# Kernel optimization log

Measured on AMD Instinct MI355X. Metric: run time of the kernel, lower is better.

## Reference

```python
import jax, jax.numpy as jnp
import numpy as np

H = 1024          # hidden_size
I = 2048          # intermediate_size (per routed expert; shared uses I*num_shared)
E = 8             # num_routed_experts
B, S = 2, 1024


def setup_inputs() -> dict:
    key = jax.random.key(0)
    ks = jax.random.split(key, 8)
    sc_h = 1.0 / np.sqrt(H)
    sc_i = 1.0 / np.sqrt(I)
    return {
        "hidden_states": jax.random.normal(ks[0], (B, S, H), jnp.float32),
        "gate_w": jax.random.normal(ks[1], (H, E), jnp.float32) * sc_h,      # router
        "sh_gate": jax.random.normal(ks[2], (H, I), jnp.float32) * sc_h,     # shared SwiGLU
        "sh_up": jax.random.normal(ks[3], (H, I), jnp.float32) * sc_h,
        "sh_down": jax.random.normal(ks[4], (I, H), jnp.float32) * sc_i,
        "rt_gate": jax.random.normal(ks[5], (E, H, I), jnp.float32) * sc_h,  # stacked routed experts
        "rt_up": jax.random.normal(ks[6], (E, H, I), jnp.float32) * sc_h,
        "rt_down": jax.random.normal(ks[7], (E, I, H), jnp.float32) * sc_i,
    }


def _swiglu(x, wg, wu, wd):
    return (jax.nn.silu(x @ wg) * (x @ wu)) @ wd


def reference(hidden_states, gate_w, sh_gate, sh_up, sh_down, rt_gate, rt_up, rt_down):
    b, s, h = hidden_states.shape
    x = hidden_states.reshape(-1, h)                      # [T, H]
    logits = x @ gate_w                                   # [T, E]
    # top-1 routing: score = sigmoid(max logit), expert = argmax
    top_val = jnp.max(logits, axis=-1, keepdims=True)     # [T, 1]
    top_id = jnp.argmax(logits, axis=-1)                  # [T]
    score = jax.nn.sigmoid(top_val)
    xs = x * score                                        # scale tokens BEFORE expert (Llama4)
    # exact dense-masked equivalent of sort/dispatch/per-expert SwiGLU/scatter-combine:
    # every expert is applied to all tokens, then the one-hot mask selects the
    # assigned expert's output per token (identical math to ragged dispatch).
    g = jnp.einsum('th,ehi->eti', xs, rt_gate)            # [E, T, I]
    u = jnp.einsum('th,ehi->eti', xs, rt_up)
    act = jax.nn.silu(g) * u
    y = jnp.einsum('eti,eih->eth', act, rt_down)          # [E, T, H]
    onehot = jax.nn.one_hot(top_id, E, dtype=x.dtype)     # [T, E]
    routed = jnp.einsum('eth,te->th', y, onehot)          # [T, H]
    shared = _swiglu(x, sh_gate, sh_up, sh_down)          # [T, H]
    return (shared + routed).reshape(b, s, h)
```

## Files before the change

kernel.cpp:

```cpp
#include <hip/hip_runtime.h>
#include <cstdint>
#include <cstddef>

#define T_TOK 2048
#define HDIM  1024
#define IDIM  2048
#define NEXP  8

#define BM 128
#define BK 32
#define BN2 64
#define MAXPAD 3072
#define SH_TILES 16
#define RT_TILES 24

typedef __attribute__((ext_vector_type(8))) short short8;
typedef __attribute__((ext_vector_type(4))) short short4v;
typedef __attribute__((ext_vector_type(4))) float float4v;

__device__ __forceinline__ short f2bf(float f) {
  uint32_t u = __float_as_uint(f);
  u += 0x7fffu + ((u >> 16) & 1u);
  return (short)(u >> 16);
}

__device__ __forceinline__ void gload_lds16(const void* g, void* l) {
  __builtin_amdgcn_global_load_lds(
      (const __attribute__((address_space(1))) uint32_t*)g,
      (__attribute__((address_space(3))) uint32_t*)l, 16, 0, 0);
}

__device__ __forceinline__ int swz(int c) { return c ^ ((c >> 4) & 3); }


__global__ __launch_bounds__(256) void zero_init(int* __restrict__ counts,
                                                 int* __restrict__ perm) {
  int i = threadIdx.x;
  if (i < NEXP) counts[i] = 0;
  for (int p = i; p < MAXPAD; p += 256) perm[p] = 0;
}

__global__ __launch_bounds__(256) void router_kernel(
    const float* __restrict__ x, const float* __restrict__ gw,
    short* __restrict__ xbf, short* __restrict__ xsbf,
    int* __restrict__ expert_id, int* __restrict__ slot,
    int* __restrict__ counts) {
  int wv = threadIdx.x >> 6, lane = threadIdx.x & 63;
  int t = blockIdx.x * 4 + wv;
  const float* xr = x + (size_t)t * HDIM;
  float4v xv[4];
  float lg[NEXP];
#pragma unroll
  for (int e = 0; e < NEXP; e++) lg[e] = 0.f;
#pragma unroll
  for (int p = 0; p < 4; p++) {
    xv[p] = *(const float4v*)(xr + p * 256 + lane * 4);
#pragma unroll
    for (int c = 0; c < 4; c++) {
      int h = p * 256 + lane * 4 + c;
      float4v g0 = *(const float4v*)(gw + (size_t)h * NEXP);
      float4v g1 = *(const float4v*)(gw + (size_t)h * NEXP + 4);
      float xc = xv[p][c];
      lg[0] += xc * g0[0]; lg[1] += xc * g0[1];
      lg[2] += xc * g0[2]; lg[3] += xc * g0[3];
      lg[4] += xc * g1[0]; lg[5] += xc * g1[1];
      lg[6] += xc * g1[2]; lg[7] += xc * g1[3];
    }
  }
#pragma unroll
  for (int ofs = 1; ofs < 64; ofs <<= 1) {
#pragma unroll
    for (int e = 0; e < NEXP; e++) lg[e] += __shfl_xor(lg[e], ofs, 64);
  }
  int be = 0;
  float bv = lg[0];
#pragma unroll
  for (int e = 1; e < NEXP; e++) {
    if (lg[e] > bv) { bv = lg[e]; be = e; }
  }
  float score = 1.f / (1.f + __expf(-bv));
  if (lane == 0) {
    expert_id[t] = be;
    slot[t] = atomicAdd(&counts[be], 1);
  }
#pragma unroll
  for (int p = 0; p < 4; p++) {
    short4v b, bs;
#pragma unroll
    for (int c = 0; c < 4; c++) {
      b[c] = f2bf(xv[p][c]);
      bs[c] = f2bf(xv[p][c] * score);
    }
    *(short4v*)(xbf + (size_t)t * HDIM + p * 256 + lane * 4) = b;
    *(short4v*)(xsbf + (size_t)t * HDIM + p * 256 + lane * 4) = bs;
  }
}

__global__ void prefix_kernel(const int* __restrict__ counts, int* __restrict__ pad_off) {
  if (threadIdx.x == 0 && blockIdx.x == 0) {
    int run = 0;
    for (int e = 0; e < NEXP; e++) {
      pad_off[e] = run;
      run += (counts[e] + BM - 1) & ~(BM - 1);
    }
    pad_off[NEXP] = run;
  }
}

__global__ __launch_bounds__(256) void build_perm(
    const int* __restrict__ expert_id, const int* __restrict__ slot,
    const int* __restrict__ pad_off, int* __restrict__ perm) {
  int t = blockIdx.x * 256 + threadIdx.x;
  int e = expert_id[t];
  perm[pad_off[e] + slot[t]] = t;
}


__global__ __launch_bounds__(256) void transpose_w1(
    const float* __restrict__ shg, const float* __restrict__ shu,
    const float* __restrict__ rtg, const float* __restrict__ rtu,
    short* __restrict__ shg_t, short* __restrict__ shu_t,
    short* __restrict__ rtg_t, short* __restrict__ rtu_t) {
  __shared__ __align__(16) short t[64][66];
  int z = blockIdx.z;
  const float *s0, *s1;
  short *d0, *d1;
  if (z == 0) { s0 = shg; s1 = shu; d0 = shg_t; d1 = shu_t; }
  else {
    size_t o = (size_t)(z - 1) * HDIM * IDIM;
    s0 = rtg + o; s1 = rtu + o; d0 = rtg_t + o; d1 = rtu_t + o;
  }
  const int R = HDIM, C = IDIM;
  int r0 = blockIdx.y * 64, c0 = blockIdx.x * 64;
  int tid = threadIdx.x;
  int tr = tid >> 4, tc = (tid & 15) * 4;
  int oc = tid >> 2, rs = (tid & 3) * 16;
#pragma unroll
  for (int pass = 0; pass < 2; pass++) {
    const float* s = pass ? s1 : s0;
    short* d = pass ? d1 : d0;
    if (pass) __syncthreads();
#pragma unroll
    for (int i = 0; i < 4; i++) {
      float4v v = *(const float4v*)(s + (size_t)(r0 + tr + i * 16) * C + c0 + tc);
      int w0 = (int)(unsigned short)f2bf(v[0]) | ((int)f2bf(v[1]) << 16);
      int w1 = (int)(unsigned short)f2bf(v[2]) | ((int)f2bf(v[3]) << 16);
      int* p = (int*)&t[tr + i * 16][tc];
      p[0] = w0;
      p[1] = w1;
    }
    __syncthreads();
    short8 o0, o1;
#pragma unroll
    for (int j = 0; j < 8; j++) { o0[j] = t[rs + j][oc]; o1[j] = t[rs + 8 + j][oc]; }
    short* dp = d + (size_t)(c0 + oc) * R + r0 + rs;
    *(short8*)dp = o0;
    *(short8*)(dp + 8) = o1;
  }
}

__global__ __launch_bounds__(256) void transpose_w2(
    const float* __restrict__ shd, const float* __restrict__ rtd,
    short* __restrict__ shd_t, short* __restrict__ rtd_t) {
  __shared__ __align__(16) short t[64][66];
  int z = blockIdx.z;
  const float* s = (z == 0) ? shd : rtd + (size_t)(z - 1) * IDIM * HDIM;
  short* d = (z == 0) ? shd_t : rtd_t + (size_t)(z - 1) * IDIM * HDIM;
  const int R = IDIM, C = HDIM;
  int r0 = blockIdx.y * 64, c0 = blockIdx.x * 64;
  int tid = threadIdx.x;
  int tr = tid >> 4, tc = (tid & 15) * 4;
  int oc = tid >> 2, rs = (tid & 3) * 16;
#pragma unroll
  for (int i = 0; i < 4; i++) {
    float4v v = *(const float4v*)(s + (size_t)(r0 + tr + i * 16) * C + c0 + tc);
    int w0 = (int)(unsigned short)f2bf(v[0]) | ((int)f2bf(v[1]) << 16);
    int w1 = (int)(unsigned short)f2bf(v[2]) | ((int)f2bf(v[3]) << 16);
    int* p = (int*)&t[tr + i * 16][tc];
    p[0] = w0;
    p[1] = w1;
  }
  __syncthreads();
  short8 o0, o1;
#pragma unroll
  for (int j = 0; j < 8; j++) { o0[j] = t[rs + j][oc]; o1[j] = t[rs + 8 + j][oc]; }
  short* dp = d + (size_t)(c0 + oc) * R + r0 + rs;
  *(short8*)dp = o0;
  *(short8*)(dp + 8) = o1;
}


__global__ __launch_bounds__(256) void gemm1_swiglu(
    const short* __restrict__ xbf, const short* __restrict__ xsbf,
    const short* __restrict__ shg_t, const short* __restrict__ shu_t,
    const short* __restrict__ rtg_t, const short* __restrict__ rtu_t,
    short* __restrict__ act_sh, short* __restrict__ act_rt,
    const int* __restrict__ pad_off, const int* __restrict__ perm) {
  __shared__ __align__(1024) short sA[BM * BK];
  __shared__ __align__(1024) short sBg[BM * BK];
  __shared__ __align__(1024) short sBu[BM * BK];
  int tid = threadIdx.x, lane = tid & 63, wv = tid >> 6;
  int C0 = blockIdx.x * 128;
  int y = blockIdx.y;
  const short *A, *Bg, *Bu;
  short* act;
  int R0;
  bool routed = (y >= SH_TILES);
  if (!routed) {
    A = xbf; Bg = shg_t; Bu = shu_t; act = act_sh; R0 = y * BM;
  } else {
    R0 = (y - SH_TILES) * BM;
    if (R0 >= pad_off[NEXP]) return;
    int e = 0;
    while (pad_off[e + 1] <= R0) e++;
    size_t o = (size_t)e * HDIM * IDIM;
    A = xsbf; Bg = rtg_t + o; Bu = rtu_t + o; act = act_rt;
  }
  int c0 = swz(tid), c1 = swz(tid + 256);
  int r0c = c0 >> 2, r1c = c1 >> 2;
  int ar0 = routed ? perm[R0 + r0c] : R0 + r0c;
  int ar1 = routed ? perm[R0 + r1c] : R0 + r1c;
  size_t gA0 = (size_t)ar0 * HDIM + (c0 & 3) * 8;
  size_t gA1 = (size_t)ar1 * HDIM + (c1 & 3) * 8;
  size_t gB0 = (size_t)(C0 + r0c) * HDIM + (c0 & 3) * 8;
  size_t gB1 = (size_t)(C0 + r1c) * HDIM + (c1 & 3) * 8;
  short* lds0 = (short*)nullptr;
  (void)lds0;
  short* lA0 = sA + tid * 8;  short* lA1 = sA + (tid + 256) * 8;
  short* lG0 = sBg + tid * 8; short* lG1 = sBg + (tid + 256) * 8;
  short* lU0 = sBu + tid * 8; short* lU1 = sBu + (tid + 256) * 8;

  float4v accg[4][4], accu[4][4];
  float4v z4 = {0.f, 0.f, 0.f, 0.f};
#pragma unroll
  for (int i = 0; i < 4; i++)
#pragma unroll
    for (int j = 0; j < 4; j++) { accg[i][j] = z4; accu[i][j] = z4; }

  const int wrow = (wv >> 1) * 64, wcol = (wv & 1) * 64;
  const int mrow = lane & 15, h4 = lane >> 4;
  int aoff[4], boff[4];
#pragma unroll
  for (int i = 0; i < 4; i++)
    aoff[i] = swz(((wrow + i * 16 + mrow) << 2) + h4) * 8;
#pragma unroll
  for (int j = 0; j < 4; j++)
    boff[j] = swz(((wcol + j * 16 + mrow) << 2) + h4) * 8;

  for (int k0 = 0; k0 < HDIM; k0 += BK) {
    __syncthreads();
    gload_lds16(A + gA0 + k0, lA0);
    gload_lds16(A + gA1 + k0, lA1);
    gload_lds16(Bg + gB0 + k0, lG0);
    gload_lds16(Bg + gB1 + k0, lG1);
    gload_lds16(Bu + gB0 + k0, lU0);
    gload_lds16(Bu + gB1 + k0, lU1);
    __syncthreads();
    short8 af[4], bg[4], bu[4];
#pragma unroll
    for (int i = 0; i < 4; i++) af[i] = *(const short8*)(sA + aoff[i]);
#pragma unroll
    for (int j = 0; j < 4; j++) {
      bg[j] = *(const short8*)(sBg + boff[j]);
      bu[j] = *(const short8*)(sBu + boff[j]);
    }
#pragma unroll
    for (int i = 0; i < 4; i++)
#pragma unroll
      for (int j = 0; j < 4; j++) {
        accg[i][j] = __builtin_amdgcn_mfma_f32_16x16x32_bf16(af[i], bg[j], accg[i][j], 0, 0, 0);
        accu[i][j] = __builtin_amdgcn_mfma_f32_16x16x32_bf16(af[i], bu[j], accu[i][j], 0, 0, 0);
      }
  }
  int qrow = h4 * 4, col = mrow;
#pragma unroll
  for (int i = 0; i < 4; i++)
#pragma unroll
    for (int j = 0; j < 4; j++)
#pragma unroll
      for (int r = 0; r < 4; r++) {
        int row = R0 + wrow + i * 16 + qrow + r;
        int c = C0 + wcol + j * 16 + col;
        float g = accg[i][j][r], u = accu[i][j][r];
        float sv = g / (1.f + __expf(-g)) * u;
        act[(size_t)row * IDIM + c] = f2bf(sv);
      }
}


__global__ __launch_bounds__(256) void gemm2_down(
    const short* __restrict__ act_sh, const short* __restrict__ act_rt,
    const short* __restrict__ shd_t, const short* __restrict__ rtd_t,
    float* __restrict__ out, float* __restrict__ rt_out,
    const int* __restrict__ pad_off, const int* __restrict__ counts,
    const int* __restrict__ perm) {
  __shared__ __align__(1024) short sA[BM * BK];
  __shared__ __align__(1024) short sB[BN2 * BK];
  int tid = threadIdx.x, lane = tid & 63, wv = tid >> 6;
  int C0 = blockIdx.x * BN2;
  int y = blockIdx.y;
  const short *A, *Bd;
  int R0, e = 0;
  bool routed = (y >= SH_TILES);
  if (!routed) {
    A = act_sh; Bd = shd_t; R0 = y * BM;
  } else {
    R0 = (y - SH_TILES) * BM;
    if (R0 >= pad_off[NEXP]) return;
    while (pad_off[e + 1] <= R0) e++;
    A = act_rt; Bd = rtd_t + (size_t)e * IDIM * HDIM;
  }
  int c0 = swz(tid), c1 = swz(tid + 256);
  size_t gA0 = (size_t)(R0 + (c0 >> 2)) * IDIM + (c0 & 3) * 8;
  size_t gA1 = (size_t)(R0 + (c1 >> 2)) * IDIM + (c1 & 3) * 8;
  size_t gB0 = (size_t)(C0 + (c0 >> 2)) * IDIM + (c0 & 3) * 8;
  short* lA0 = sA + tid * 8;
  short* lA1 = sA + (tid + 256) * 8;
  short* lB0 = sB + tid * 8;

  float4v acc[2][4];
  float4v z4 = {0.f, 0.f, 0.f, 0.f};
#pragma unroll
  for (int i = 0; i < 2; i++)
#pragma unroll
    for (int j = 0; j < 4; j++) acc[i][j] = z4;

  const int wrow = wv * 32;
  const int mrow = lane & 15, h4 = lane >> 4;
  int aoff[2], boff[4];
#pragma unroll
  for (int i = 0; i < 2; i++)
    aoff[i] = swz(((wrow + i * 16 + mrow) << 2) + h4) * 8;
#pragma unroll
  for (int j = 0; j < 4; j++)
    boff[j] = swz(((j * 16 + mrow) << 2) + h4) * 8;

  for (int k0 = 0; k0 < IDIM; k0 += BK) {
    __syncthreads();
    gload_lds16(A + gA0 + k0, lA0);
    gload_lds16(A + gA1 + k0, lA1);
    gload_lds16(Bd + gB0 + k0, lB0);
    __syncthreads();
    short8 af[2], bf4[4];
#pragma unroll
    for (int i = 0; i < 2; i++) af[i] = *(const short8*)(sA + aoff[i]);
#pragma unroll
    for (int j = 0; j < 4; j++) bf4[j] = *(const short8*)(sB + boff[j]);
#pragma unroll
    for (int i = 0; i < 2; i++)
#pragma unroll
      for (int j = 0; j < 4; j++)
        acc[i][j] = __builtin_amdgcn_mfma_f32_16x16x32_bf16(af[i], bf4[j], acc[i][j], 0, 0, 0);
  }
  int qrow = h4 * 4, col = mrow;
#pragma unroll
  for (int i = 0; i < 2; i++)
#pragma unroll
    for (int j = 0; j < 4; j++)
#pragma unroll
      for (int r = 0; r < 4; r++) {
        int row = R0 + wrow + i * 16 + qrow + r;
        int c = C0 + j * 16 + col;
        float v = acc[i][j][r];
        if (!routed) {
          out[(size_t)row * HDIM + c] = v;
        } else if (row - pad_off[e] < counts[e]) {
          rt_out[(size_t)perm[row] * HDIM + c] = v;
        }
      }
}

__global__ __launch_bounds__(256) void add_routed(float* __restrict__ out,
                                                  const float* __restrict__ rt_out) {
  size_t i = ((size_t)blockIdx.x * 256 + threadIdx.x) * 4;
  float4v a = *(const float4v*)(out + i);
  float4v b = *(const float4v*)(rt_out + i);
  a[0] += b[0]; a[1] += b[1]; a[2] += b[2]; a[3] += b[3];
  *(float4v*)(out + i) = a;
}


extern "C" void kernel_launch(void* const* d_in, const int* in_sizes, int n_in,
                              void* d_out, int out_size, void* d_ws, size_t ws_size,
                              hipStream_t stream) {
  const float* x       = (const float*)d_in[0];
  const float* gate_w  = (const float*)d_in[1];
  const float* sh_gate = (const float*)d_in[2];
  const float* sh_up   = (const float*)d_in[3];
  const float* sh_down = (const float*)d_in[4];
  const float* rt_gate = (const float*)d_in[5];
  const float* rt_up   = (const float*)d_in[6];
  const float* rt_down = (const float*)d_in[7];
  float* out = (float*)d_out;

  char* w = (char*)d_ws;
  const size_t MB = 1024 * 1024;
  short* xbf    = (short*)(w + 0 * MB);
  short* xsbf   = (short*)(w + 4 * MB);
  short* act_sh = (short*)(w + 8 * MB);
  short* act_rt = (short*)(w + 16 * MB);
  float* rt_out = (float*)(w + 28 * MB);
  short* shg_t  = (short*)(w + 36 * MB);
  short* shu_t  = (short*)(w + 40 * MB);
  short* shd_t  = (short*)(w + 44 * MB);
  short* rtg_t  = (short*)(w + 48 * MB);
  short* rtu_t  = (short*)(w + 80 * MB);
  short* rtd_t  = (short*)(w + 112 * MB);
  int* ints     = (int*)(w + 144 * MB);
  int* counts    = ints;
  int* pad_off   = ints + 8;
  int* expert_id = ints + 32;
  int* slot      = ints + 32 + 2048;
  int* perm      = ints + 32 + 4096;

  zero_init<<<1, 256, 0, stream>>>(counts, perm);
  router_kernel<<<T_TOK / 4, 256, 0, stream>>>(x, gate_w, xbf, xsbf, expert_id, slot, counts);
  prefix_kernel<<<1, 64, 0, stream>>>(counts, pad_off);
  build_perm<<<T_TOK / 256, 256, 0, stream>>>(expert_id, slot, pad_off, perm);

  transpose_w1<<<dim3(IDIM / 64, HDIM / 64, 1 + NEXP), 256, 0, stream>>>(
      sh_gate, sh_up, rt_gate, rt_up, shg_t, shu_t, rtg_t, rtu_t);
  transpose_w2<<<dim3(HDIM / 64, IDIM / 64, 1 + NEXP), 256, 0, stream>>>(
      sh_down, rt_down, shd_t, rtd_t);

  gemm1_swiglu<<<dim3(IDIM / 128, SH_TILES + RT_TILES), 256, 0, stream>>>(
      xbf, xsbf, shg_t, shu_t, rtg_t, rtu_t, act_sh, act_rt, pad_off, perm);

  gemm2_down<<<dim3(HDIM / BN2, SH_TILES + RT_TILES), 256, 0, stream>>>(
      act_sh, act_rt, shd_t, rtd_t, out, rt_out, pad_off, counts, perm);

  add_routed<<<(T_TOK * HDIM) / (256 * 4), 256, 0, stream>>>(out, rt_out);
}
```

Baseline: 438.5 us.

## Double-buffer LDS tiles in both GEMM kernels and retune swizzle

Both GEMM kernels now keep two LDS buffers per operand. Each iteration issues the global-to-LDS prefetch of the next K slice before running MFMA on the current one, so there is one barrier per iteration instead of two. The aim is to overlap global load latency with matrix math. The LDS swizzle changes from XOR on bits 4-5 to bits 3-4 to reduce bank conflicts on fragment reads. In exchange, LDS use doubles (48KB per block in gemm1), which may lower occupancy, and the last iteration issues a redundant dummy load.

After: 453.6 us. 1.03x slower.

```diff
diff --git a/kernel.cpp b/kernel.cpp
--- a/kernel.cpp
+++ b/kernel.cpp
@@ -30,7 +30,7 @@
       (__attribute__((address_space(3))) uint32_t*)l, 16, 0, 0);
 }
 
-__device__ __forceinline__ int swz(int c) { return c ^ ((c >> 4) & 3); }
+__device__ __forceinline__ int swz(int c) { return c ^ ((c >> 3) & 3); }
 
 
 __global__ __launch_bounds__(256) void zero_init(int* __restrict__ counts,
@@ -196,9 +196,9 @@
     const short* __restrict__ rtg_t, const short* __restrict__ rtu_t,
     short* __restrict__ act_sh, short* __restrict__ act_rt,
     const int* __restrict__ pad_off, const int* __restrict__ perm) {
-  __shared__ __align__(1024) short sA[BM * BK];
-  __shared__ __align__(1024) short sBg[BM * BK];
-  __shared__ __align__(1024) short sBu[BM * BK];
+  __shared__ __align__(1024) short sA[2][4096];
+  __shared__ __align__(1024) short sBg[2][4096];
+  __shared__ __align__(1024) short sBu[2][4096];
   int tid = threadIdx.x, lane = tid & 63, wv = tid >> 6;
   int C0 = blockIdx.x * 128;
   int y = blockIdx.y;
@@ -217,18 +217,13 @@
     A = xsbf; Bg = rtg_t + o; Bu = rtu_t + o; act = act_rt;
   }
   int c0 = swz(tid), c1 = swz(tid + 256);
-  int r0c = c0 >> 2, r1c = c1 >> 2;
-  int ar0 = routed ? perm[R0 + r0c] : R0 + r0c;
-  int ar1 = routed ? perm[R0 + r1c] : R0 + r1c;
+  int ar0 = routed ? perm[R0 + (c0 >> 2)] : R0 + (c0 >> 2);
+  int ar1 = routed ? perm[R0 + (c1 >> 2)] : R0 + (c1 >> 2);
   size_t gA0 = (size_t)ar0 * HDIM + (c0 & 3) * 8;
   size_t gA1 = (size_t)ar1 * HDIM + (c1 & 3) * 8;
-  size_t gB0 = (size_t)(C0 + r0c) * HDIM + (c0 & 3) * 8;
-  size_t gB1 = (size_t)(C0 + r1c) * HDIM + (c1 & 3) * 8;
-  short* lds0 = (short*)nullptr;
-  (void)lds0;
-  short* lA0 = sA + tid * 8;  short* lA1 = sA + (tid + 256) * 8;
-  short* lG0 = sBg + tid * 8; short* lG1 = sBg + (tid + 256) * 8;
-  short* lU0 = sBu + tid * 8; short* lU1 = sBu + (tid + 256) * 8;
+  size_t gB0 = (size_t)(C0 + (c0 >> 2)) * HDIM + (c0 & 3) * 8;
+  size_t gB1 = (size_t)(C0 + (c1 >> 2)) * HDIM + (c1 & 3) * 8;
+  int l0 = tid * 8, l1 = (tid + 256) * 8;
 
   float4v accg[4][4], accu[4][4];
   float4v z4 = {0.f, 0.f, 0.f, 0.f};
@@ -242,27 +237,36 @@
   int aoff[4], boff[4];
 #pragma unroll
   for (int i = 0; i < 4; i++)
-    aoff[i] = swz(((wrow + i * 16 + mrow) << 2) + h4) * 8;
+    aoff[i] = swz(((wrow + i * 16 + mrow) << 2) | h4) * 8;
 #pragma unroll
   for (int j = 0; j < 4; j++)
-    boff[j] = swz(((wcol + j * 16 + mrow) << 2) + h4) * 8;
-
-  for (int k0 = 0; k0 < HDIM; k0 += BK) {
+    boff[j] = swz(((wcol + j * 16 + mrow) << 2) | h4) * 8;
+
+#define STAGE1(b, k)                                \
+  do {                                              \
+    gload_lds16(A + gA0 + (k), &sA[b][l0]);         \
+    gload_lds16(A + gA1 + (k), &sA[b][l1]);         \
+    gload_lds16(Bg + gB0 + (k), &sBg[b][l0]);       \
+    gload_lds16(Bg + gB1 + (k), &sBg[b][l1]);       \
+    gload_lds16(Bu + gB0 + (k), &sBu[b][l0]);       \
+    gload_lds16(Bu + gB1 + (k), &sBu[b][l1]);       \
+  } while (0)
+
+  STAGE1(0, 0);
+  for (int s = 0; s < 32; s++) {
     __syncthreads();
-    gload_lds16(A + gA0 + k0, lA0);
-    gload_lds16(A + gA1 + k0, lA1);
-    gload_lds16(Bg + gB0 + k0, lG0);
-    gload_lds16(Bg + gB1 + k0, lG1);
-    gload_lds16(Bu + gB0 + k0, lU0);
-    gload_lds16(Bu + gB1 + k0, lU1);
-    __syncthreads();
+    int kn = (s < 31) ? (s + 1) * BK : 0;
+    STAGE1((s + 1) & 1, kn);
+    const short* pA = sA[s & 1];
+    const short* pG = sBg[s & 1];
+    const short* pU = sBu[s & 1];
     short8 af[4], bg[4], bu[4];
 #pragma unroll
-    for (int i = 0; i < 4; i++) af[i] = *(const short8*)(sA + aoff[i]);
+    for (int i = 0; i < 4; i++) af[i] = *(const short8*)(pA + aoff[i]);
 #pragma unroll
     for (int j = 0; j < 4; j++) {
-      bg[j] = *(const short8*)(sBg + boff[j]);
-      bu[j] = *(const short8*)(sBu + boff[j]);
+      bg[j] = *(const short8*)(pG + boff[j]);
+      bu[j] = *(const short8*)(pU + boff[j]);
     }
 #pragma unroll
     for (int i = 0; i < 4; i++)
@@ -272,6 +276,7 @@
         accu[i][j] = __builtin_amdgcn_mfma_f32_16x16x32_bf16(af[i], bu[j], accu[i][j], 0, 0, 0);
       }
   }
+#undef STAGE1
   int qrow = h4 * 4, col = mrow;
 #pragma unroll
   for (int i = 0; i < 4; i++)
@@ -294,8 +299,8 @@
     float* __restrict__ out, float* __restrict__ rt_out,
     const int* __restrict__ pad_off, const int* __restrict__ counts,
     const int* __restrict__ perm) {
-  __shared__ __align__(1024) short sA[BM * BK];
-  __shared__ __align__(1024) short sB[BN2 * BK];
+  __shared__ __align__(1024) short sA[2][4096];
+  __shared__ __align__(1024) short sB[2][2048];
   int tid = threadIdx.x, lane = tid & 63, wv = tid >> 6;
   int C0 = blockIdx.x * BN2;
   int y = blockIdx.y;
@@ -314,9 +319,7 @@
   size_t gA0 = (size_t)(R0 + (c0 >> 2)) * IDIM + (c0 & 3) * 8;
   size_t gA1 = (size_t)(R0 + (c1 >> 2)) * IDIM + (c1 & 3) * 8;
   size_t gB0 = (size_t)(C0 + (c0 >> 2)) * IDIM + (c0 & 3) * 8;
-  short* lA0 = sA + tid * 8;
-  short* lA1 = sA + (tid + 256) * 8;
-  short* lB0 = sB + tid * 8;
+  int l0 = tid * 8, l1 = (tid + 256) * 8;
 
   float4v acc[2][4];
   float4v z4 = {0.f, 0.f, 0.f, 0.f};
@@ -330,28 +333,37 @@
   int aoff[2], boff[4];
 #pragma unroll
   for (int i = 0; i < 2; i++)
-    aoff[i] = swz(((wrow + i * 16 + mrow) << 2) + h4) * 8;
+    aoff[i] = swz(((wrow + i * 16 + mrow) << 2) | h4) * 8;
 #pragma unroll
   for (int j = 0; j < 4; j++)
-    boff[j] = swz(((j * 16 + mrow) << 2) + h4) * 8;
-
-  for (int k0 = 0; k0 < IDIM; k0 += BK) {
+    boff[j] = swz(((j * 16 + mrow) << 2) | h4) * 8;
+
+#define STAGE2(b, k)                                \
+  do {                                              \
+    gload_lds16(A + gA0 + (k), &sA[b][l0]);         \
+    gload_lds16(A + gA1 + (k), &sA[b][l1]);         \
+    gload_lds16(Bd + gB0 + (k), &sB[b][l0]);        \
+  } while (0)
+
+  STAGE2(0, 0);
+  for (int s = 0; s < 64; s++) {
     __syncthreads();
-    gload_lds16(A + gA0 + k0, lA0);
-    gload_lds16(A + gA1 + k0, lA1);
-    gload_lds16(Bd + gB0 + k0, lB0);
-    __syncthreads();
+    int kn = (s < 63) ? (s + 1) * BK : 0;
+    STAGE2((s + 1) & 1, kn);
+    const short* pA = sA[s & 1];
+    const short* pB = sB[s & 1];
     short8 af[2], bf4[4];
 #pragma unroll
-    for (int i = 0; i < 2; i++) af[i] = *(const short8*)(sA + aoff[i]);
-#pragma unroll
-    for (int j = 0; j < 4; j++) bf4[j] = *(const short8*)(sB + boff[j]);
+    for (int i = 0; i < 2; i++) af[i] = *(const short8*)(pA + aoff[i]);
+#pragma unroll
+    for (int j = 0; j < 4; j++) bf4[j] = *(const short8*)(pB + boff[j]);
 #pragma unroll
     for (int i = 0; i < 2; i++)
 #pragma unroll
       for (int j = 0; j < 4; j++)
         acc[i][j] = __builtin_amdgcn_mfma_f32_16x16x32_bf16(af[i], bf4[j], acc[i][j], 0, 0, 0);
   }
+#undef STAGE2
   int qrow = h4 * 4, col = mrow;
 #pragma unroll
   for (int i = 0; i < 2; i++)
```

## Load GEMM operands directly from global into registers with double buffering

Applied to the files above, without the earlier changes.

Both GEMM kernels stop staging A/B tiles in LDS and instead have each wave load its MFMA fragments straight from global memory into registers, with a two-set register double buffer that overlaps the next k-step's loads with the current MFMAs. The barriers per k-step go away. gemm2 also grows from a 128x64 to a 128x128 tile with 4x4 fragments per wave, and launch bounds gain occupancy hints. In exchange, operands that LDS used to share across waves are now re-read from global/L2 by every wave, and register pressure rises.

Result: slower. 593.2 us (+35.3%).

```diff
diff --git a/kernel.cpp b/kernel.cpp
--- a/kernel.cpp
+++ b/kernel.cpp
@@ -9,7 +9,6 @@
 
 #define BM 128
 #define BK 32
-#define BN2 64
 #define MAXPAD 3072
 #define SH_TILES 16
 #define RT_TILES 24
@@ -23,14 +22,6 @@
   u += 0x7fffu + ((u >> 16) & 1u);
   return (short)(u >> 16);
 }
-
-__device__ __forceinline__ void gload_lds16(const void* g, void* l) {
-  __builtin_amdgcn_global_load_lds(
-      (const __attribute__((address_space(1))) uint32_t*)g,
-      (__attribute__((address_space(3))) uint32_t*)l, 16, 0, 0);
-}
-
-__device__ __forceinline__ int swz(int c) { return c ^ ((c >> 4) & 3); }
 
 
 __global__ __launch_bounds__(256) void zero_init(int* __restrict__ counts,
@@ -190,15 +181,12 @@
 }
 
 
-__global__ __launch_bounds__(256) void gemm1_swiglu(
+__global__ __launch_bounds__(256, 2) void gemm1_swiglu(
     const short* __restrict__ xbf, const short* __restrict__ xsbf,
     const short* __restrict__ shg_t, const short* __restrict__ shu_t,
     const short* __restrict__ rtg_t, const short* __restrict__ rtu_t,
     short* __restrict__ act_sh, short* __restrict__ act_rt,
     const int* __restrict__ pad_off, const int* __restrict__ perm) {
-  __shared__ __align__(1024) short sA[BM * BK];
-  __shared__ __align__(1024) short sBg[BM * BK];
-  __shared__ __align__(1024) short sBu[BM * BK];
   int tid = threadIdx.x, lane = tid & 63, wv = tid >> 6;
   int C0 = blockIdx.x * 128;
   int y = blockIdx.y;
@@ -216,62 +204,64 @@
     size_t o = (size_t)e * HDIM * IDIM;
     A = xsbf; Bg = rtg_t + o; Bu = rtu_t + o; act = act_rt;
   }
-  int c0 = swz(tid), c1 = swz(tid + 256);
-  int r0c = c0 >> 2, r1c = c1 >> 2;
-  int ar0 = routed ? perm[R0 + r0c] : R0 + r0c;
-  int ar1 = routed ? perm[R0 + r1c] : R0 + r1c;
-  size_t gA0 = (size_t)ar0 * HDIM + (c0 & 3) * 8;
-  size_t gA1 = (size_t)ar1 * HDIM + (c1 & 3) * 8;
-  size_t gB0 = (size_t)(C0 + r0c) * HDIM + (c0 & 3) * 8;
-  size_t gB1 = (size_t)(C0 + r1c) * HDIM + (c1 & 3) * 8;
-  short* lds0 = (short*)nullptr;
-  (void)lds0;
-  short* lA0 = sA + tid * 8;  short* lA1 = sA + (tid + 256) * 8;
-  short* lG0 = sBg + tid * 8; short* lG1 = sBg + (tid + 256) * 8;
-  short* lU0 = sBu + tid * 8; short* lU1 = sBu + (tid + 256) * 8;
-
-  float4v accg[4][4], accu[4][4];
-  float4v z4 = {0.f, 0.f, 0.f, 0.f};
-#pragma unroll
-  for (int i = 0; i < 4; i++)
-#pragma unroll
-    for (int j = 0; j < 4; j++) { accg[i][j] = z4; accu[i][j] = z4; }
-
   const int wrow = (wv >> 1) * 64, wcol = (wv & 1) * 64;
   const int mrow = lane & 15, h4 = lane >> 4;
   int aoff[4], boff[4];
 #pragma unroll
+  for (int i = 0; i < 4; i++) {
+    int r = R0 + wrow + i * 16 + mrow;
+    int gr = routed ? perm[r] : r;
+    aoff[i] = gr * (HDIM * 2) + h4 * 16;
+  }
+#pragma unroll
+  for (int j = 0; j < 4; j++)
+    boff[j] = (C0 + wcol + j * 16 + mrow) * (HDIM * 2) + h4 * 16;
+
+  float4v accg[4][4], accu[4][4];
+  float4v z4 = {0.f, 0.f, 0.f, 0.f};
+#pragma unroll
   for (int i = 0; i < 4; i++)
-    aoff[i] = swz(((wrow + i * 16 + mrow) << 2) + h4) * 8;
-#pragma unroll
-  for (int j = 0; j < 4; j++)
-    boff[j] = swz(((wcol + j * 16 + mrow) << 2) + h4) * 8;
-
-  for (int k0 = 0; k0 < HDIM; k0 += BK) {
-    __syncthreads();
-    gload_lds16(A + gA0 + k0, lA0);
-    gload_lds16(A + gA1 + k0, lA1);
-    gload_lds16(Bg + gB0 + k0, lG0);
-    gload_lds16(Bg + gB1 + k0, lG1);
-    gload_lds16(Bu + gB0 + k0, lU0);
-    gload_lds16(Bu + gB1 + k0, lU1);
-    __syncthreads();
-    short8 af[4], bg[4], bu[4];
-#pragma unroll
-    for (int i = 0; i < 4; i++) af[i] = *(const short8*)(sA + aoff[i]);
-#pragma unroll
-    for (int j = 0; j < 4; j++) {
-      bg[j] = *(const short8*)(sBg + boff[j]);
-      bu[j] = *(const short8*)(sBu + boff[j]);
-    }
-#pragma unroll
-    for (int i = 0; i < 4; i++)
-#pragma unroll
-      for (int j = 0; j < 4; j++) {
-        accg[i][j] = __builtin_amdgcn_mfma_f32_16x16x32_bf16(af[i], bg[j], accg[i][j], 0, 0, 0);
-        accu[i][j] = __builtin_amdgcn_mfma_f32_16x16x32_bf16(af[i], bu[j], accu[i][j], 0, 0, 0);
-      }
-  }
+#pragma unroll
+    for (int j = 0; j < 4; j++) { accg[i][j] = z4; accu[i][j] = z4; }
+
+  const char* Ab = (const char*)A;
+  const char* Gb = (const char*)Bg;
+  const char* Ub = (const char*)Bu;
+
+#define LD1(set, kb)                                                      \
+  do {                                                                    \
+    _Pragma("unroll") for (int i = 0; i < 4; i++)                         \
+        a##set[i] = *(const short8*)(Ab + aoff[i] + (kb));                \
+    _Pragma("unroll") for (int j = 0; j < 4; j++) {                       \
+      g##set[j] = *(const short8*)(Gb + boff[j] + (kb));                  \
+      u##set[j] = *(const short8*)(Ub + boff[j] + (kb));                  \
+    }                                                                     \
+  } while (0)
+
+#define FMA1(set)                                                         \
+  do {                                                                    \
+    _Pragma("unroll") for (int i = 0; i < 4; i++)                         \
+        _Pragma("unroll") for (int j = 0; j < 4; j++) {                   \
+      accg[i][j] = __builtin_amdgcn_mfma_f32_16x16x32_bf16(               \
+          a##set[i], g##set[j], accg[i][j], 0, 0, 0);                     \
+      accu[i][j] = __builtin_amdgcn_mfma_f32_16x16x32_bf16(               \
+          a##set[i], u##set[j], accu[i][j], 0, 0, 0);                     \
+    }                                                                     \
+  } while (0)
+
+  short8 a0[4], g0[4], u0[4], a1[4], g1[4], u1[4];
+  LD1(0, 0);
+  for (int s = 0; s < 32; s += 2) {
+    int k1 = (s + 1) * (BK * 2);
+    int k2 = ((s + 2) * (BK * 2)) & (HDIM * 2 - 1);
+    LD1(1, k1);
+    FMA1(0);
+    LD1(0, k2);
+    FMA1(1);
+  }
+#undef LD1
+#undef FMA1
+
   int qrow = h4 * 4, col = mrow;
 #pragma unroll
   for (int i = 0; i < 4; i++)
@@ -288,16 +278,14 @@
 }
 
 
-__global__ __launch_bounds__(256) void gemm2_down(
+__global__ __launch_bounds__(256, 3) void gemm2_down(
     const short* __restrict__ act_sh, const short* __restrict__ act_rt,
     const short* __restrict__ shd_t, const short* __restrict__ rtd_t,
     float* __restrict__ out, float* __restrict__ rt_out,
     const int* __restrict__ pad_off, const int* __restrict__ counts,
     const int* __restrict__ perm) {
-  __shared__ __align__(1024) short sA[BM * BK];
-  __shared__ __align__(1024) short sB[BN2 * BK];
   int tid = threadIdx.x, lane = tid & 63, wv = tid >> 6;
-  int C0 = blockIdx.x * BN2;
+  int C0 = blockIdx.x * 128;
   int y = blockIdx.y;
   const short *A, *Bd;
   int R0, e = 0;
@@ -310,57 +298,64 @@
     while (pad_off[e + 1] <= R0) e++;
     A = act_rt; Bd = rtd_t + (size_t)e * IDIM * HDIM;
   }
-  int c0 = swz(tid), c1 = swz(tid + 256);
-  size_t gA0 = (size_t)(R0 + (c0 >> 2)) * IDIM + (c0 & 3) * 8;
-  size_t gA1 = (size_t)(R0 + (c1 >> 2)) * IDIM + (c1 & 3) * 8;
-  size_t gB0 = (size_t)(C0 + (c0 >> 2)) * IDIM + (c0 & 3) * 8;
-  short* lA0 = sA + tid * 8;
-  short* lA1 = sA + (tid + 256) * 8;
-  short* lB0 = sB + tid * 8;
-
-  float4v acc[2][4];
+  const int wrow = (wv >> 1) * 64, wcol = (wv & 1) * 64;
+  const int mrow = lane & 15, h4 = lane >> 4;
+  int aoff[4], boff[4];
+#pragma unroll
+  for (int i = 0; i < 4; i++)
+    aoff[i] = (R0 + wrow + i * 16 + mrow) * (IDIM * 2) + h4 * 16;
+#pragma unroll
+  for (int j = 0; j < 4; j++)
+    boff[j] = (C0 + wcol + j * 16 + mrow) * (IDIM * 2) + h4 * 16;
+
+  float4v acc[4][4];
   float4v z4 = {0.f, 0.f, 0.f, 0.f};
 #pragma unroll
-  for (int i = 0; i < 2; i++)
+  for (int i = 0; i < 4; i++)
 #pragma unroll
     for (int j = 0; j < 4; j++) acc[i][j] = z4;
 
-  const int wrow = wv * 32;
-  const int mrow = lane & 15, h4 = lane >> 4;
-  int aoff[2], boff[4];
-#pragma unroll
-  for (int i = 0; i < 2; i++)
-    aoff[i] = swz(((wrow + i * 16 + mrow) << 2) + h4) * 8;
-#pragma unroll
-  for (int j = 0; j < 4; j++)
-    boff[j] = swz(((j * 16 + mrow) << 2) + h4) * 8;
-
-  for (int k0 = 0; k0 < IDIM; k0 += BK) {
-    __syncthreads();
-    gload_lds16(A + gA0 + k0, lA0);
-    gload_lds16(A + gA1 + k0, lA1);
-    gload_lds16(Bd + gB0 + k0, lB0);
-    __syncthreads();
-    short8 af[2], bf4[4];
-#pragma unroll
-    for (int i = 0; i < 2; i++) af[i] = *(const short8*)(sA + aoff[i]);
-#pragma unroll
-    for (int j = 0; j < 4; j++) bf4[j] = *(const short8*)(sB + boff[j]);
-#pragma unroll
-    for (int i = 0; i < 2; i++)
-#pragma unroll
-      for (int j = 0; j < 4; j++)
-        acc[i][j] = __builtin_amdgcn_mfma_f32_16x16x32_bf16(af[i], bf4[j], acc[i][j], 0, 0, 0);
-  }
+  const char* Ab = (const char*)A;
+  const char* Bb = (const char*)Bd;
+
+#define LD2(set, kb)                                                      \
+  do {                                                                    \
+    _Pragma("unroll") for (int i = 0; i < 4; i++)                         \
+        a##set[i] = *(const short8*)(Ab + aoff[i] + (kb));                \
+    _Pragma("unroll") for (int j = 0; j < 4; j++)                         \
+        b##set[j] = *(const short8*)(Bb + boff[j] + (kb));                \
+  } while (0)
+
+#define FMA2(set)                                                         \
+  do {                                                                    \
+    _Pragma("unroll") for (int i = 0; i < 4; i++)                         \
+        _Pragma("unroll") for (int j = 0; j < 4; j++)                     \
+            acc[i][j] = __builtin_amdgcn_mfma_f32_16x16x32_bf16(          \
+                a##set[i], b##set[j], acc[i][j], 0, 0, 0);                \
+  } while (0)
+
+  short8 a0[4], b0[4], a1[4], b1[4];
+  LD2(0, 0);
+  for (int s = 0; s < 64; s += 2) {
+    int k1 = (s + 1) * (BK * 2);
+    int k2 = ((s + 2) * (BK * 2)) & (IDIM * 2 - 1);
+    LD2(1, k1);
+    FMA2(0);
+    LD2(0, k2);
+    FMA2(1);
+  }
+#undef LD2
+#undef FMA2
+
   int qrow = h4 * 4, col = mrow;
 #pragma unroll
-  for (int i = 0; i < 2; i++)
+  for (int i = 0; i < 4; i++)
 #pragma unroll
     for (int j = 0; j < 4; j++)
 #pragma unroll
       for (int r = 0; r < 4; r++) {
         int row = R0 + wrow + i * 16 + qrow + r;
-        int c = C0 + j * 16 + col;
+        int c = C0 + wcol + j * 16 + col;
         float v = acc[i][j][r];
         if (!routed) {
           out[(size_t)row * HDIM + c] = v;
@@ -426,7 +421,7 @@
   gemm1_swiglu<<<dim3(IDIM / 128, SH_TILES + RT_TILES), 256, 0, stream>>>(
       xbf, xsbf, shg_t, shu_t, rtg_t, rtu_t, act_sh, act_rt, pad_off, perm);
 
-  gemm2_down<<<dim3(HDIM / BN2, SH_TILES + RT_TILES), 256, 0, stream>>>(
+  gemm2_down<<<dim3(HDIM / 128, SH_TILES + RT_TILES), 256, 0, stream>>>(
       act_sh, act_rt, shd_t, rtd_t, out, rt_out, pad_off, counts, perm);
 
   add_routed<<<(T_TOK * HDIM) / (256 * 4), 256, 0, stream>>>(out, rt_out);
```
